# Kernel tuning notes

Hardware: AMD Instinct MI355X
Metric: run time of the kernel (lower is better)

## Reference

```python
import jax, jax.numpy as jnp
import numpy as np

B, PS, E, A, EMB, D, V, LC, TCAP = 128, 14, 2048, 512, 512, 512, 10000, 128, 26
T = TCAP - 1  # max decode length


def setup_inputs() -> dict:
    key = jax.random.key(0)
    ks = jax.random.split(key, 16)
    g = lambda k, shape: jax.random.normal(k, shape, jnp.float32) * 0.02
    cap_len = jax.random.randint(ks[2], (B, 1), 2, TCAP + 1).at[0, 0].set(TCAP)
    return {
        "encoder_out": jax.random.normal(ks[0], (B, PS, PS, E), jnp.float32),
        "encoded_captions": jax.random.randint(ks[1], (B, TCAP), 0, V),
        "caption_lengths": cap_len,
        "length_class": jax.random.randint(ks[3], (B,), 0, 3),
        "W_enc_att": g(ks[4], (E, A)), "b_enc_att": jnp.zeros((A,), jnp.float32),
        "W_dec_att": g(ks[5], (D, A)), "b_dec_att": jnp.zeros((A,), jnp.float32),
        "w_full_att": g(ks[6], (A,)), "b_full_att": jnp.zeros((), jnp.float32),
        "W_init_h": g(ks[7], (E, D)), "b_init_h": jnp.zeros((D,), jnp.float32),
        "W_init_c": g(ks[8], (E, D)), "b_init_c": jnp.zeros((D,), jnp.float32),
        "W_fbeta": g(ks[9], (D, E)), "b_fbeta": jnp.zeros((E,), jnp.float32),
        "emb_table": jax.random.uniform(ks[10], (V, EMB), jnp.float32, -0.1, 0.1),
        "lc_table": jax.random.uniform(ks[11], (3, LC), jnp.float32, -0.1, 0.1),
        "W_fc": jax.random.uniform(ks[12], (D, V), jnp.float32, -0.1, 0.1),
        "b_fc": jnp.zeros((V,), jnp.float32),
        "W_ih": g(ks[13], (EMB + E + LC, 4 * D)), "b_ih": jnp.zeros((4 * D,), jnp.float32),
        "W_hh": g(ks[14], (D, 4 * D)), "b_hh": jnp.zeros((4 * D,), jnp.float32),
    }


def reference(encoder_out, encoded_captions, caption_lengths, length_class,
              W_enc_att, b_enc_att, W_dec_att, b_dec_att, w_full_att, b_full_att,
              W_init_h, b_init_h, W_init_c, b_init_c, W_fbeta, b_fbeta,
              emb_table, lc_table, W_fc, b_fc, W_ih, b_ih, W_hh, b_hh):
    enc = encoder_out.reshape(B, -1, E)                      # [B, P, E]
    cap_len = caption_lengths[:, 0]
    sort_ind = jnp.argsort(-cap_len)                          # descending by length
    enc = enc[sort_ind]
    caps = encoded_captions[sort_ind]
    style = lc_table[length_class[sort_ind]]                  # [B, LC]
    dec_len = cap_len[sort_ind] - 1                           # [B]

    embs = emb_table[caps]                                    # [B, TCAP, EMB]
    mean_enc = enc.mean(axis=1)
    h0 = mean_enc @ W_init_h + b_init_h
    c0 = mean_enc @ W_init_c + b_init_c
    # encoder side of attention is time-invariant: precompute once
    att1 = jnp.einsum('bpe,ea->bpa', enc, W_enc_att) + b_enc_att

    def step(carry, xs):
        h, c = carry
        t, emb_t = xs
        att2 = h @ W_dec_att + b_dec_att
        e = jnp.einsum('bpa,a->bp', jax.nn.relu(att1 + att2[:, None, :]), w_full_att) + b_full_att
        alpha = jax.nn.softmax(e, axis=1)                     # [B, P]
        awe = jnp.einsum('bpe,bp->be', enc, alpha)
        gate = jax.nn.sigmoid(h @ W_fbeta + b_fbeta)
        x = jnp.concatenate([emb_t, style, gate * awe], axis=1)
        gates = x @ W_ih + b_ih + h @ W_hh + b_hh             # [B, 4D], order i,f,g,o
        i, f, g, o = jnp.split(gates, 4, axis=1)
        c_new = jax.nn.sigmoid(f) * c + jax.nn.sigmoid(i) * jnp.tanh(g)
        h_new = jax.nn.sigmoid(o) * jnp.tanh(c_new)
        preds = h_new @ W_fc + b_fc                           # dropout is identity in eval
        m = (t < dec_len)[:, None]                            # active sequences at step t
        return ((jnp.where(m, h_new, h), jnp.where(m, c_new, c)),
                (jnp.where(m, preds, 0.0), jnp.where(m, alpha, 0.0)))

    ts = jnp.arange(T)
    emb_seq = jnp.swapaxes(embs[:, :T, :], 0, 1)              # [T, B, EMB]
    _, (preds, alphas) = jax.lax.scan(step, (h0, c0), (ts, emb_seq))
    predictions = jnp.swapaxes(preds, 0, 1)                   # [B, T, V]
    alphas = jnp.swapaxes(alphas, 0, 1)                       # [B, T, P]
    return predictions, caps, dec_len, alphas, sort_ind
```

## Files before the change

kernel.cpp:

```cpp
#include <hip/hip_runtime.h>
#include <math.h>

constexpr int kB   = 128;
constexpr int kP   = 196;
constexpr int kE   = 2048;
constexpr int kA   = 512;
constexpr int kEMB = 512;
constexpr int kD   = 512;
constexpr int kV   = 10000;
constexpr int kLC  = 128;
constexpr int kTCAP= 26;
constexpr int kT   = 25;
constexpr int kX   = kEMB + kLC + kE;
constexpr int kXH  = kX + kD;
constexpr int kN3  = kV + kA + kE;
constexpr int kBIG = 1 << 30;
constexpr int KZ   = 5;

typedef __attribute__((ext_vector_type(8))) short bf8;
typedef __attribute__((ext_vector_type(4))) float f4;

__device__ inline float b2f(ushort u) { return __uint_as_float(((unsigned)u) << 16); }
__device__ inline ushort f2b(float f) {
    unsigned u = __float_as_uint(f);
    return (ushort)((u + 0x7fffu + ((u >> 16) & 1u)) >> 16);
}

#define SWZ(r, k) ((((r) * 32) + (k)) ^ (((r) & 7) << 3))

__global__ __launch_bounds__(128) void sort_setup(
    const int* __restrict__ caplen, const int* __restrict__ caps_in,
    const int* __restrict__ lclass, const float* __restrict__ lc_table,
    int* __restrict__ sort_ind, int* __restrict__ declen, int* __restrict__ caps_i,
    float* __restrict__ style,
    float* __restrict__ out_caps, float* __restrict__ out_declen,
    float* __restrict__ out_sortind)
{
    __shared__ int lens[kB];
    __shared__ int sind[kB];
    int i = threadIdx.x;
    lens[i] = caplen[i];
    __syncthreads();
    int li = lens[i];
    int r = 0;
    for (int j = 0; j < kB; j++) {
        int lj = lens[j];
        if (lj > li || (lj == li && j < i)) r++;
    }
    sind[r] = i;
    sort_ind[r] = i;
    out_sortind[r] = (float)i;
    __syncthreads();
    int orig = sind[i];
    int dl = lens[orig] - 1;
    declen[i] = dl;
    out_declen[i] = (float)dl;
    for (int t = 0; t < kTCAP; t++) {
        int cv = caps_in[orig * kTCAP + t];
        caps_i[i * kTCAP + t] = cv;
        out_caps[i * kTCAP + t] = (float)cv;
    }
    int lcl = lclass[orig];
    for (int k = 0; k < kLC; k++) style[i * kLC + k] = lc_table[lcl * kLC + k];
}

__global__ __launch_bounds__(256) void tcvt_kernel(
    const float* __restrict__ src, int ldsrc, int K, int N,
    ushort* __restrict__ dst, long long ldd)
{
    __shared__ float tile[32][33];
    int k0 = blockIdx.y * 32, n0 = blockIdx.x * 32;
    int tx = threadIdx.x & 31, ty = threadIdx.x >> 5;
    #pragma unroll
    for (int j = 0; j < 4; j++) {
        int k = k0 + ty + j * 8, n = n0 + tx;
        tile[ty + j * 8][tx] = (k < K && n < N) ? src[(long long)k * ldsrc + n] : 0.f;
    }
    __syncthreads();
    #pragma unroll
    for (int j = 0; j < 4; j++) {
        int n = n0 + ty + j * 8, k = k0 + tx;
        if (n < N && k < K) dst[(long long)n * ldd + k] = f2b(tile[tx][ty + j * 8]);
    }
}

__global__ __launch_bounds__(256) void bias_setup_kernel(
    const float* __restrict__ b_fc, const float* __restrict__ b_dec,
    const float* __restrict__ b_fb, const float* __restrict__ b_ih0,
    const float* __restrict__ b_ic0, const float* __restrict__ b_ih,
    const float* __restrict__ b_hh,
    float* __restrict__ bias3, float* __restrict__ bias_hc, float* __restrict__ gbias)
{
    int idx = blockIdx.x * 256 + threadIdx.x;
    if (idx < kN3) {
        float v;
        if (idx < kV) v = b_fc[idx];
        else if (idx < kV + kA) v = b_dec[idx - kV];
        else v = b_fb[idx - kV - kA];
        bias3[idx] = v;
    } else if (idx < kN3 + 1024) {
        int i = idx - kN3;
        bias_hc[i] = (i < 512) ? b_ih0[i] : b_ic0[i - 512];
    } else if (idx < kN3 + 1024 + 2048) {
        int i = idx - kN3 - 1024;
        gbias[i] = b_ih[i] + b_hh[i];
    }
}

__global__ __launch_bounds__(256) void enc_cvt_kernel(
    const float* __restrict__ enc, const int* __restrict__ sort_ind,
    ushort* __restrict__ enc_bf)
{
    long long idx4 = (long long)blockIdx.x * 256 + threadIdx.x;
    if (idx4 >= (long long)kB * kP * kE / 4) return;
    int r = (int)(idx4 >> 9);
    int cc = ((int)idx4 & 511) * 4;
    int b = r / kP, p = r - b * kP;
    long long srow = (long long)sort_ind[b] * kP + p;
    float4 v = *(const float4*)(enc + srow * kE + cc);
    ushort4 o; o.x = f2b(v.x); o.y = f2b(v.y); o.z = f2b(v.z); o.w = f2b(v.w);
    *(ushort4*)(enc_bf + (long long)r * kE + cc) = o;
}

__global__ __launch_bounds__(256) void mean_enc_kernel(
    const float* __restrict__ encf, const ushort* __restrict__ encb, int use_bf,
    const int* __restrict__ sort_ind, float* __restrict__ me)
{
    int idx = blockIdx.x * 256 + threadIdx.x;
    int b = idx >> 11, e = idx & 2047;
    float s = 0.f;
    if (use_bf) {
        const ushort* base = encb + (long long)b * kP * kE + e;
        #pragma unroll 4
        for (int p = 0; p < kP; p++) s += b2f(base[(long long)p * kE]);
    } else {
        const float* base = encf + (long long)sort_ind[b] * kP * kE + e;
        #pragma unroll 4
        for (int p = 0; p < kP; p++) s += base[(long long)p * kE];
    }
    me[idx] = s * (1.0f / 196.0f);
}

__global__ __launch_bounds__(256) void gemm2(
    const void* __restrict__ Am, int lda, int a_bf16,
    const ushort* __restrict__ Bt, int ldbt,
    const float* __restrict__ bias,
    void* __restrict__ out1, long long ldc1, int c1_bf16,
    int split1, float* __restrict__ out2, long long ldc2,
    int split2, float* __restrict__ out3, long long ldc3,
    const int* __restrict__ declen, int t, int pred_mode,
    int M, int N, int K, long long zstride)
{
    __shared__ short As[64 * 32];
    __shared__ short Bs[128 * 32];
    int tid = threadIdx.x;
    int lane = tid & 63, w = tid >> 6, quad = lane >> 4, l16 = lane & 15;
    int m0 = blockIdx.y * 64, n0 = blockIdx.x * 128;

    f4 acc[8];
    #pragma unroll
    for (int i = 0; i < 8; i++) acc[i] = (f4){0.f, 0.f, 0.f, 0.f};

    int a_r = tid >> 2;
    int a_kc = (tid & 3) * 8;
    long long a_row = m0 + a_r;
    const float*  a_srcf = (const float*)Am  + a_row * (long long)lda + a_kc;
    const ushort* a_srcb = (const ushort*)Am + a_row * (long long)lda + a_kc;

    int b_r = tid >> 1;
    int b_kc = (tid & 1) * 16;
    bool bvalid = (n0 + b_r) < N;
    const ushort* b_src = Bt + (long long)(n0 + b_r) * ldbt + b_kc;

    int kpb = K / (int)gridDim.z;
    int kbeg = (int)blockIdx.z * kpb, kend = kbeg + kpb;

    float4 af0 = make_float4(0.f, 0.f, 0.f, 0.f), af1 = af0;
    uint4 au, bu0, bu1;
    au.x = au.y = au.z = au.w = 0u; bu0 = au; bu1 = au;

    if (a_bf16) au = *(const uint4*)(a_srcb + kbeg);
    else { af0 = *(const float4*)(a_srcf + kbeg); af1 = *(const float4*)(a_srcf + kbeg + 4); }
    if (bvalid) { bu0 = *(const uint4*)(b_src + kbeg); bu1 = *(const uint4*)(b_src + kbeg + 8); }

    for (int k0 = kbeg; k0 < kend; k0 += 32) {
        __syncthreads();
        if (a_bf16) {
            *(uint4*)&As[SWZ(a_r, a_kc)] = au;
        } else {
            uint4 pk; ushort* pp = (ushort*)&pk;
            pp[0] = f2b(af0.x); pp[1] = f2b(af0.y); pp[2] = f2b(af0.z); pp[3] = f2b(af0.w);
            pp[4] = f2b(af1.x); pp[5] = f2b(af1.y); pp[6] = f2b(af1.z); pp[7] = f2b(af1.w);
            *(uint4*)&As[SWZ(a_r, a_kc)] = pk;
        }
        *(uint4*)&Bs[SWZ(b_r, b_kc)]     = bu0;
        *(uint4*)&Bs[SWZ(b_r, b_kc + 8)] = bu1;
        int kn = k0 + 32;
        if (kn < kend) {
            if (a_bf16) au = *(const uint4*)(a_srcb + kn);
            else { af0 = *(const float4*)(a_srcf + kn); af1 = *(const float4*)(a_srcf + kn + 4); }
            if (bvalid) { bu0 = *(const uint4*)(b_src + kn); bu1 = *(const uint4*)(b_src + kn + 8); }
        }
        __syncthreads();
        bf8 a = *(const bf8*)&As[SWZ(w * 16 + l16, quad * 8)];
        #pragma unroll
        for (int nt = 0; nt < 8; nt++) {
            bf8 b = *(const bf8*)&Bs[SWZ(nt * 16 + l16, quad * 8)];
            acc[nt] = __builtin_amdgcn_mfma_f32_16x16x32_bf16(a, b, acc[nt], 0, 0, 0);
        }
    }

    long long zoff = (long long)blockIdx.z * zstride;
    #pragma unroll
    for (int nt = 0; nt < 8; nt++) {
        int cn = n0 + nt * 16 + l16;
        if (cn >= N) continue;
        float bv = bias ? bias[cn] : 0.f;
        #pragma unroll
        for (int reg = 0; reg < 4; reg++) {
            int rr = m0 + w * 16 + quad * 4 + reg;
            float v = acc[nt][reg] + bv;
            if (cn < split1) {
                long long idx;
                if (pred_mode) {
                    int bb = rr & 127, tt = rr >> 7;
                    if (tt >= declen[bb]) v = 0.f;
                    idx = ((long long)bb * kT + tt) * ldc1 + cn;
                } else {
                    if (declen && t >= declen[rr]) v = 0.f;
                    idx = (long long)rr * ldc1 + cn + zoff;
                }
                if (c1_bf16) ((ushort*)out1)[idx] = f2b(v);
                else         ((float*)out1)[idx] = v;
            } else if (cn < split2) {
                out2[(long long)rr * ldc2 + (cn - split1)] = v;
            } else {
                out3[(long long)rr * ldc3 + (cn - split2)] = v;
            }
        }
    }
}

__global__ __launch_bounds__(256) void gemm_big(
    const ushort* __restrict__ A, int lda,
    const ushort* __restrict__ Bt, int ldbt,
    const float* __restrict__ bias,
    void* __restrict__ out1, long long ldc1, int c1_bf16,
    const int* __restrict__ declen, int pred_mode,
    int M, int N, int K)
{
    __shared__ short As[128 * 32];
    __shared__ short Bs[128 * 32];
    unsigned nwg = gridDim.x * gridDim.y;
    unsigned lin = blockIdx.y * gridDim.x + blockIdx.x;
    unsigned q = nwg >> 3, rm = nwg & 7;
    unsigned xcd = lin & 7, loc = lin >> 3;
    unsigned swz = (xcd < rm ? xcd * (q + 1) : rm * (q + 1) + (xcd - rm) * q) + loc;
    int bx = (int)(swz % gridDim.x), by = (int)(swz / gridDim.x);
    int m0 = by * 128, n0 = bx * 128;

    int tid = threadIdx.x;
    int lane = tid & 63, w = tid >> 6, quad = lane >> 4, l16 = lane & 15;
    int wr = w >> 1, wc = w & 1;

    f4 acc[4][4];
    #pragma unroll
    for (int m = 0; m < 4; m++)
        #pragma unroll
        for (int n = 0; n < 4; n++) acc[m][n] = (f4){0.f, 0.f, 0.f, 0.f};

    bool wact = true;
    if (pred_mode) wact = declen[wr * 64] > (m0 >> 7);

    int s_r = tid >> 1, s_kc = (tid & 1) * 16;
    const ushort* a_src = A + (long long)(m0 + s_r) * lda + s_kc;
    bool bval = (n0 + s_r) < N;
    const ushort* b_src = Bt + (long long)(n0 + s_r) * ldbt + s_kc;

    uint4 au0, au1, bu0, bu1;
    au0.x = au0.y = au0.z = au0.w = 0u; au1 = au0; bu0 = au0; bu1 = au0;
    au0 = *(const uint4*)(a_src);
    au1 = *(const uint4*)(a_src + 8);
    if (bval) { bu0 = *(const uint4*)(b_src); bu1 = *(const uint4*)(b_src + 8); }

    for (int k0 = 0; k0 < K; k0 += 32) {
        __syncthreads();
        *(uint4*)&As[SWZ(s_r, s_kc)]     = au0;
        *(uint4*)&As[SWZ(s_r, s_kc + 8)] = au1;
        *(uint4*)&Bs[SWZ(s_r, s_kc)]     = bu0;
        *(uint4*)&Bs[SWZ(s_r, s_kc + 8)] = bu1;
        int kn = k0 + 32;
        if (kn < K) {
            au0 = *(const uint4*)(a_src + kn);
            au1 = *(const uint4*)(a_src + kn + 8);
            if (bval) { bu0 = *(const uint4*)(b_src + kn); bu1 = *(const uint4*)(b_src + kn + 8); }
        }
        __syncthreads();
        if (wact) {
            bf8 af[4], bfr[4];
            #pragma unroll
            for (int m = 0; m < 4; m++)
                af[m] = *(const bf8*)&As[SWZ(wr * 64 + m * 16 + l16, quad * 8)];
            #pragma unroll
            for (int n = 0; n < 4; n++)
                bfr[n] = *(const bf8*)&Bs[SWZ(wc * 64 + n * 16 + l16, quad * 8)];
            #pragma unroll
            for (int m = 0; m < 4; m++)
                #pragma unroll
                for (int n = 0; n < 4; n++)
                    acc[m][n] = __builtin_amdgcn_mfma_f32_16x16x32_bf16(af[m], bfr[n], acc[m][n], 0, 0, 0);
        }
    }

    #pragma unroll
    for (int n = 0; n < 4; n++) {
        int cn = n0 + wc * 64 + n * 16 + l16;
        if (cn >= N) continue;
        float bv = bias ? bias[cn] : 0.f;
        #pragma unroll
        for (int m = 0; m < 4; m++) {
            #pragma unroll
            for (int reg = 0; reg < 4; reg++) {
                int rr = m0 + wr * 64 + m * 16 + quad * 4 + reg;
                float v = acc[m][n][reg] + bv;
                long long idx;
                if (pred_mode) {
                    int bb = rr & 127, tt = rr >> 7;
                    if (tt >= declen[bb]) v = 0.f;
                    idx = ((long long)bb * kT + tt) * ldc1 + cn;
                } else {
                    idx = (long long)rr * ldc1 + cn;
                }
                if (c1_bf16) ((ushort*)out1)[idx] = f2b(v);
                else         ((float*)out1)[idx] = v;
            }
        }
    }
}

__global__ __launch_bounds__(512) void attn_awe_kernel(
    const ushort* __restrict__ att1, const float* __restrict__ att2,
    const float* __restrict__ w_full, const float* __restrict__ b_full,
    const float* __restrict__ encf, const ushort* __restrict__ encb, int use_bf,
    const int* __restrict__ sort_ind, const float* __restrict__ gate,
    const int* __restrict__ caps_i, int t,
    const float* __restrict__ emb_table, const float* __restrict__ style,
    float* __restrict__ xh, float* __restrict__ alphas_out,
    const int* __restrict__ declen, const int* __restrict__ smap)
{
    int b = blockIdx.y;
    int half = blockIdx.x;
    int ob = smap ? smap[b] : b;
    __shared__ float al[kP];
    __shared__ float red1[8], red2[8];
    int tid = threadIdx.x, wave = tid >> 6, lane = tid & 63;

    float a2r[8], wfr[8];
    {
        const float4* ap = (const float4*)(att2 + (long long)b * kA + lane * 8);
        *(float4*)&a2r[0] = ap[0]; *(float4*)&a2r[4] = ap[1];
        const float4* wp = (const float4*)(w_full + lane * 8);
        *(float4*)&wfr[0] = wp[0]; *(float4*)&wfr[4] = wp[1];
    }
    float bfull = b_full[0];
    const ushort* a1 = att1 + (long long)ob * kP * kA + lane * 8;
    for (int i0 = 0; i0 < 25; i0 += 4) {
        uint4 u[4]; int pv[4];
        #pragma unroll
        for (int j = 0; j < 4; j++) {
            int i = i0 + j, p = wave + 8 * i;
            pv[j] = (i < 25 && p < kP) ? p : -1;
            if (pv[j] >= 0) u[j] = *(const uint4*)(a1 + (long long)pv[j] * kA);
        }
        #pragma unroll
        for (int j = 0; j < 4; j++) {
            if (pv[j] < 0) continue;
            const unsigned* uw = (const unsigned*)&u[j];
            float s = 0.f;
            #pragma unroll
            for (int q = 0; q < 4; q++) {
                unsigned x = uw[q];
                float v0 = b2f((ushort)(x & 0xffffu)) + a2r[2 * q];
                float v1 = b2f((ushort)(x >> 16))     + a2r[2 * q + 1];
                s += fmaxf(v0, 0.f) * wfr[2 * q] + fmaxf(v1, 0.f) * wfr[2 * q + 1];
            }
            #pragma unroll
            for (int off = 32; off; off >>= 1) s += __shfl_down(s, off);
            if (lane == 0) al[pv[j]] = s + bfull;
        }
    }
    __syncthreads();

    float e = (tid < kP) ? al[tid] : -1e30f;
    float wm = e;
    for (int off = 32; off; off >>= 1) wm = fmaxf(wm, __shfl_down(wm, off));
    if (lane == 0) red1[wave] = wm;
    __syncthreads();
    float gm = red1[0];
    #pragma unroll
    for (int i = 1; i < 8; i++) gm = fmaxf(gm, red1[i]);
    float ex = (tid < kP) ? expf(e - gm) : 0.f;
    float sw = ex;
    for (int off = 32; off; off >>= 1) sw += __shfl_down(sw, off);
    if (lane == 0) red2[wave] = sw;
    __syncthreads();
    float S = red2[0];
    #pragma unroll
    for (int i = 1; i < 8; i++) S += red2[i];
    float a = ex / S;
    __syncthreads();
    if (tid < kP) {
        al[tid] = a;
        if (half == 0)
            alphas_out[((long long)b * kT + t) * kP + tid] = (t < declen[b]) ? a : 0.f;
    }
    __syncthreads();

    if (half == 1 && tid < 160) {
        int tok = caps_i[b * kTCAP + t];
        float4 v;
        if (tid < 128) v = *(const float4*)(emb_table + (long long)tok * kEMB + tid * 4);
        else           v = *(const float4*)(style + b * kLC + (tid - 128) * 4);
        *(float4*)(xh + (long long)b * kXH + tid * 4) = v;
    }

    int c0 = half * 1024 + tid * 2;
    float s0 = 0.f, s1 = 0.f;
    if (use_bf) {
        const ushort* base = encb + (long long)b * kP * kE + c0;
        #pragma unroll 4
        for (int p = 0; p < kP; p++) {
            unsigned uu = *(const unsigned*)(base + (long long)p * kE);
            float ap = al[p];
            s0 += b2f((ushort)(uu & 0xffffu)) * ap;
            s1 += b2f((ushort)(uu >> 16))     * ap;
        }
    } else {
        const float* base = encf + (long long)sort_ind[b] * kP * kE + c0;
        #pragma unroll 4
        for (int p = 0; p < kP; p++) {
            float2 v = *(const float2*)(base + (long long)p * kE);
            float ap = al[p];
            s0 += v.x * ap; s1 += v.y * ap;
        }
    }
    float2 g = *(const float2*)(gate + (long long)b * kE + c0);
    float2 o;
    o.x = s0 / (1.f + expf(-g.x));
    o.y = s1 / (1.f + expf(-g.y));
    *(float2*)(xh + (long long)b * kXH + kEMB + kLC + c0) = o;
}

__global__ __launch_bounds__(256) void lstm_cell_kernel(
    const float* __restrict__ gpart, const float* __restrict__ gbias,
    float* __restrict__ xh, float* __restrict__ c,
    ushort* __restrict__ Hbuf, int t)
{
    int idx = blockIdx.x * 256 + threadIdx.x;
    int b = idx >> 9, d = idx & 511;
    float gi = gbias[d], gf = gbias[kD + d], gg = gbias[2 * kD + d], go = gbias[3 * kD + d];
    const float* g = gpart + (long long)b * 4 * kD + d;
    #pragma unroll
    for (int z = 0; z < KZ; z++) {
        const float* gz = g + (long long)z * kB * 4 * kD;
        gi += gz[0]; gf += gz[kD]; gg += gz[2 * kD]; go += gz[3 * kD];
    }
    float si = 1.f / (1.f + expf(-gi));
    float sf = 1.f / (1.f + expf(-gf));
    float so = 1.f / (1.f + expf(-go));
    float cn = sf * c[idx] + si * tanhf(gg);
    float hn = so * tanhf(cn);
    c[idx] = cn;
    xh[(long long)b * kXH + kX + d] = hn;
    Hbuf[((long long)t * kB + b) * kD + d] = f2b(hn);
}

extern "C" void kernel_launch(void* const* d_in, const int* in_sizes, int n_in,
                              void* d_out, int out_size, void* d_ws, size_t ws_size,
                              hipStream_t stream)
{
    const float* encoder_out  = (const float*)d_in[0];
    const int*   enc_caps     = (const int*)  d_in[1];
    const int*   cap_lengths  = (const int*)  d_in[2];
    const int*   length_class = (const int*)  d_in[3];
    const float* W_enc_att = (const float*)d_in[4];
    const float* b_enc_att = (const float*)d_in[5];
    const float* W_dec_att = (const float*)d_in[6];
    const float* b_dec_att = (const float*)d_in[7];
    const float* w_full_att = (const float*)d_in[8];
    const float* b_full_att = (const float*)d_in[9];
    const float* W_init_h = (const float*)d_in[10];
    const float* b_init_h = (const float*)d_in[11];
    const float* W_init_c = (const float*)d_in[12];
    const float* b_init_c = (const float*)d_in[13];
    const float* W_fbeta  = (const float*)d_in[14];
    const float* b_fbeta  = (const float*)d_in[15];
    const float* emb_table = (const float*)d_in[16];
    const float* lc_table  = (const float*)d_in[17];
    const float* W_fc = (const float*)d_in[18];
    const float* b_fc = (const float*)d_in[19];
    const float* W_ih = (const float*)d_in[20];
    const float* b_ih = (const float*)d_in[21];
    const float* W_hh = (const float*)d_in[22];
    const float* b_hh = (const float*)d_in[23];

    float* out = (float*)d_out;
    float* o_pred    = out;
    float* o_caps    = out + (long long)kB * kT * kV;
    float* o_declen  = o_caps + kB * kTCAP;
    float* o_alpha   = o_declen + kB;
    float* o_sortind = o_alpha + (long long)kB * kT * kP;

    float* w = (float*)d_ws;
    float* xh       = w; w += kB * kXH;
    float* c        = w; w += kB * kD;
    float* att2     = w; w += kB * kA;
    float* gate     = w; w += kB * kE;
    float* mean_enc = w; w += kB * kE;
    float* gpart    = w; w += (long long)kB * 4 * kD * KZ;
    float* style    = w; w += kB * kLC;
    float* bias3    = w; w += kN3;
    float* bias_hc  = w; w += 1024;
    float* gbias    = w; w += 2048;
    ushort* us = (ushort*)w;
    ushort* att1_bf  = us; us += (long long)kB * kP * kA;
    ushort* WencT    = us; us += (long long)kA * kE;
    ushort* WhcT     = us; us += (long long)1024 * kE;
    ushort* WcatT    = us; us += (long long)(4 * kD) * kXH;
    ushort* Wcat3T   = us; us += (long long)kN3 * kD;
    ushort* Hbuf     = us; us += (long long)kT * kB * kD;
    int* iw = (int*)us;
    int* sort_ind = iw; iw += kB;
    int* declen   = iw; iw += kB;
    int* caps_i   = iw; iw += kB * kTCAP;
    ushort* enc_bf = (ushort*)(iw + kB);

    size_t need_with_enc = ((char*)(enc_bf + (long long)kB * kP * kE)) - (char*)d_ws;
    int use_encbf = (ws_size >= need_with_enc) ? 1 : 0;

    sort_setup<<<1, 128, 0, stream>>>(cap_lengths, enc_caps, length_class, lc_table,
        sort_ind, declen, caps_i, style, o_caps, o_declen, o_sortind);

    auto tc = [&](const float* s, int ldsrc, int Kr, int Nc, ushort* d, long long ldd) {
        tcvt_kernel<<<dim3((Nc + 31) / 32, (Kr + 31) / 32), 256, 0, stream>>>(
            s, ldsrc, Kr, Nc, d, ldd);
    };
    tc(W_enc_att, kA, kE, kA, WencT, kE);
    tc(W_init_h,  kD, kE, kD, WhcT, kE);
    tc(W_init_c,  kD, kE, kD, WhcT + (long long)kD * kE, kE);
    tc(W_ih, 4 * kD, kX, 4 * kD, WcatT, kXH);
    tc(W_hh, 4 * kD, kD, 4 * kD, WcatT + kX, kXH);
    tc(W_fc,      kV, kD, kV, Wcat3T, kD);
    tc(W_dec_att, kA, kD, kA, Wcat3T + (long long)kV * kD, kD);
    tc(W_fbeta,   kE, kD, kE, Wcat3T + (long long)(kV + kA) * kD, kD);
    bias_setup_kernel<<<(kN3 + 1024 + 2048 + 255) / 256, 256, 0, stream>>>(
        b_fc, b_dec_att, b_fbeta, b_init_h, b_init_c, b_ih, b_hh, bias3, bias_hc, gbias);

    if (use_encbf) {
        enc_cvt_kernel<<<(unsigned)(((long long)kB * kP * kE / 4 + 255) / 256), 256, 0, stream>>>(
            encoder_out, sort_ind, enc_bf);
    }
    mean_enc_kernel<<<(kB * kE) / 256, 256, 0, stream>>>(
        encoder_out, enc_bf, use_encbf, sort_ind, mean_enc);

    auto g2 = [](int M, int N) { return dim3((unsigned)((N + 127) / 128), (unsigned)(M / 64)); };

    gemm2<<<g2(kB, 1024), 256, 0, stream>>>(mean_enc, kE, 0, WhcT, kE, bias_hc,
        xh + kX, kXH, 0, 512, c, kD, kBIG, nullptr, 0, nullptr, 0, 0,
        kB, 1024, kE, 0);

    if (use_encbf) {
        gemm_big<<<dim3(kA / 128, kB * kP / 128), 256, 0, stream>>>(
            enc_bf, kE, WencT, kE, b_enc_att,
            att1_bf, kA, 1, nullptr, 0, kB * kP, kA, kE);
    } else {
        gemm2<<<g2(kB * kP, kA), 256, 0, stream>>>(encoder_out, kE, 0, WencT, kE, b_enc_att,
            att1_bf, kA, 1, kBIG, nullptr, 0, kBIG, nullptr, 0, nullptr, 0, 0,
            kB * kP, kA, kE, 0);
    }

    gemm2<<<g2(kB, kA + kE), 256, 0, stream>>>(xh + kX, kXH, 0,
        Wcat3T + (long long)kV * kD, kD, bias3 + kV, att2, kA, 0,
        kA, gate, kE, kBIG, nullptr, 0, nullptr, 0, 0, kB, kA + kE, kD, 0);

    const int* smap = use_encbf ? nullptr : sort_ind;
    for (int t = 0; t < kT; t++) {
        attn_awe_kernel<<<dim3(2, kB), 512, 0, stream>>>(att1_bf, att2, w_full_att,
            b_full_att, encoder_out, enc_bf, use_encbf, sort_ind, gate, caps_i, t,
            emb_table, style, xh, o_alpha, declen, smap);
        gemm2<<<dim3((4 * kD + 127) / 128, kB / 64, KZ), 256, 0, stream>>>(
            xh, kXH, 0, WcatT, kXH, nullptr,
            gpart, 4 * kD, 0, kBIG, nullptr, 0, kBIG, nullptr, 0, nullptr, 0, 0,
            kB, 4 * kD, kXH, (long long)kB * 4 * kD);
        lstm_cell_kernel<<<(kB * kD) / 256, 256, 0, stream>>>(gpart, gbias, xh, c, Hbuf, t);
        gemm2<<<g2(kB, kA + kE), 256, 0, stream>>>(xh + kX, kXH, 0,
            Wcat3T + (long long)kV * kD, kD, bias3 + kV, att2, kA, 0,
            kA, gate, kE, kBIG, nullptr, 0, nullptr, 0, 0, kB, kA + kE, kD, 0);
    }

    gemm_big<<<dim3((kV + 127) / 128, kT * kB / 128), 256, 0, stream>>>(
        Hbuf, kD, Wcat3T, kD, bias3,
        o_pred, kV, 0, declen, 1, kT * kB, kV, kD);
}
```

Baseline: 2.737 ms.

## Transpose bf16 encoder to P-contiguous layout and keep LSTM input in bf16

Adds a kernel that transposes the bf16 encoder features into a [B, E, P] layout padded to 200 so that the per-step attention-weighted sum and the mean reduction read contiguous 16-byte vectors instead of strided scalars. The xh activation buffer also becomes bf16, which halves the A-operand traffic for the recurrent gate GEMMs and drops the fp32-to-bf16 conversion there. In exchange the code spends an extra transpose pass and more workspace, falls back to the old paths when the workspace is too small, and rounds the hidden state to bf16 before the recurrent matmul.

Measured after the change: 2.634 ms. -3.8%, faster.

```diff
diff --git a/kernel.cpp b/kernel.cpp
--- a/kernel.cpp
+++ b/kernel.cpp
@@ -3,6 +3,7 @@
 
 constexpr int kB   = 128;
 constexpr int kP   = 196;
+constexpr int kPT  = 200;
 constexpr int kE   = 2048;
 constexpr int kA   = 512;
 constexpr int kEMB = 512;
@@ -122,14 +123,43 @@
     *(ushort4*)(enc_bf + (long long)r * kE + cc) = o;
 }
 
+__global__ __launch_bounds__(256) void encT_kernel(
+    const ushort* __restrict__ enc_bf, ushort* __restrict__ enc_T)
+{
+    __shared__ ushort tile[kPT][65];
+    int b = blockIdx.y, e0 = blockIdx.x * 64;
+    int tid = threadIdx.x;
+    tile[196 + (tid >> 6)][tid & 63] = 0;
+    const ushort* src = enc_bf + (long long)b * kP * kE + e0;
+    for (int idx = tid; idx < kP * 64; idx += 256) {
+        int p = idx >> 6, j = idx & 63;
+        tile[p][j] = src[(long long)p * kE + j];
+    }
+    __syncthreads();
+    ushort* dst = enc_T + ((long long)b * kE + e0) * kPT;
+    for (int j = 0; j < 64; j++) {
+        if (tid < kPT) dst[(long long)j * kPT + tid] = tile[tid][j];
+    }
+}
+
 __global__ __launch_bounds__(256) void mean_enc_kernel(
-    const float* __restrict__ encf, const ushort* __restrict__ encb, int use_bf,
+    const float* __restrict__ encf, const ushort* __restrict__ encb,
+    const ushort* __restrict__ encT, int mode,
     const int* __restrict__ sort_ind, float* __restrict__ me)
 {
     int idx = blockIdx.x * 256 + threadIdx.x;
     int b = idx >> 11, e = idx & 2047;
     float s = 0.f;
-    if (use_bf) {
+    if (mode == 2) {
+        const ushort* base = encT + (long long)idx * kPT;
+        #pragma unroll
+        for (int i = 0; i < kPT / 8; i++) {
+            uint4 u = *(const uint4*)(base + i * 8);
+            const ushort* pu = (const ushort*)&u;
+            #pragma unroll
+            for (int j = 0; j < 8; j++) s += b2f(pu[j]);
+        }
+    } else if (mode == 1) {
         const ushort* base = encb + (long long)b * kP * kE + e;
         #pragma unroll 4
         for (int p = 0; p < kP; p++) s += b2f(base[(long long)p * kE]);
@@ -341,17 +371,18 @@
 __global__ __launch_bounds__(512) void attn_awe_kernel(
     const ushort* __restrict__ att1, const float* __restrict__ att2,
     const float* __restrict__ w_full, const float* __restrict__ b_full,
-    const float* __restrict__ encf, const ushort* __restrict__ encb, int use_bf,
+    const float* __restrict__ encf, const ushort* __restrict__ encb,
+    const ushort* __restrict__ encT, int mode,
     const int* __restrict__ sort_ind, const float* __restrict__ gate,
     const int* __restrict__ caps_i, int t,
     const float* __restrict__ emb_table, const float* __restrict__ style,
-    float* __restrict__ xh, float* __restrict__ alphas_out,
+    ushort* __restrict__ xh, float* __restrict__ alphas_out,
     const int* __restrict__ declen, const int* __restrict__ smap)
 {
     int b = blockIdx.y;
     int half = blockIdx.x;
     int ob = smap ? smap[b] : b;
-    __shared__ float al[kP];
+    __shared__ float al[kPT];
     __shared__ float red1[8], red2[8];
     int tid = threadIdx.x, wave = tid >> 6, lane = tid & 63;
 
@@ -413,6 +444,8 @@
         al[tid] = a;
         if (half == 0)
             alphas_out[((long long)b * kT + t) * kP + tid] = (t < declen[b]) ? a : 0.f;
+    } else if (tid < kPT) {
+        al[tid] = 0.f;
     }
     __syncthreads();
 
@@ -421,12 +454,29 @@
         float4 v;
         if (tid < 128) v = *(const float4*)(emb_table + (long long)tok * kEMB + tid * 4);
         else           v = *(const float4*)(style + b * kLC + (tid - 128) * 4);
-        *(float4*)(xh + (long long)b * kXH + tid * 4) = v;
+        ushort4 o; o.x = f2b(v.x); o.y = f2b(v.y); o.z = f2b(v.z); o.w = f2b(v.w);
+        *(ushort4*)(xh + (long long)b * kXH + tid * 4) = o;
     }
 
     int c0 = half * 1024 + tid * 2;
     float s0 = 0.f, s1 = 0.f;
-    if (use_bf) {
+    if (mode == 2) {
+        const ushort* r0 = encT + ((long long)b * kE + c0) * kPT;
+        const ushort* r1 = r0 + kPT;
+        #pragma unroll 5
+        for (int i = 0; i < kPT / 8; i++) {
+            uint4 ua = *(const uint4*)(r0 + i * 8);
+            uint4 ub = *(const uint4*)(r1 + i * 8);
+            f4 alo = *(const f4*)&al[i * 8];
+            f4 ahi = *(const f4*)&al[i * 8 + 4];
+            const ushort* pa = (const ushort*)&ua;
+            const ushort* pb = (const ushort*)&ub;
+            s0 += b2f(pa[0]) * alo.x + b2f(pa[1]) * alo.y + b2f(pa[2]) * alo.z + b2f(pa[3]) * alo.w;
+            s0 += b2f(pa[4]) * ahi.x + b2f(pa[5]) * ahi.y + b2f(pa[6]) * ahi.z + b2f(pa[7]) * ahi.w;
+            s1 += b2f(pb[0]) * alo.x + b2f(pb[1]) * alo.y + b2f(pb[2]) * alo.z + b2f(pb[3]) * alo.w;
+            s1 += b2f(pb[4]) * ahi.x + b2f(pb[5]) * ahi.y + b2f(pb[6]) * ahi.z + b2f(pb[7]) * ahi.w;
+        }
+    } else if (mode == 1) {
         const ushort* base = encb + (long long)b * kP * kE + c0;
         #pragma unroll 4
         for (int p = 0; p < kP; p++) {
@@ -445,15 +495,15 @@
         }
     }
     float2 g = *(const float2*)(gate + (long long)b * kE + c0);
-    float2 o;
-    o.x = s0 / (1.f + expf(-g.x));
-    o.y = s1 / (1.f + expf(-g.y));
-    *(float2*)(xh + (long long)b * kXH + kEMB + kLC + c0) = o;
+    float o0 = s0 / (1.f + expf(-g.x));
+    float o1 = s1 / (1.f + expf(-g.y));
+    unsigned pw = (unsigned)f2b(o0) | ((unsigned)f2b(o1) << 16);
+    *(unsigned*)(xh + (long long)b * kXH + kEMB + kLC + c0) = pw;
 }
 
 __global__ __launch_bounds__(256) void lstm_cell_kernel(
     const float* __restrict__ gpart, const float* __restrict__ gbias,
-    float* __restrict__ xh, float* __restrict__ c,
+    ushort* __restrict__ xh, float* __restrict__ c,
     ushort* __restrict__ Hbuf, int t)
 {
     int idx = blockIdx.x * 256 + threadIdx.x;
@@ -471,8 +521,9 @@
     float cn = sf * c[idx] + si * tanhf(gg);
     float hn = so * tanhf(cn);
     c[idx] = cn;
-    xh[(long long)b * kXH + kX + d] = hn;
-    Hbuf[((long long)t * kB + b) * kD + d] = f2b(hn);
+    ushort hb = f2b(hn);
+    xh[(long long)b * kXH + kX + d] = hb;
+    Hbuf[((long long)t * kB + b) * kD + d] = hb;
 }
 
 extern "C" void kernel_launch(void* const* d_in, const int* in_sizes, int n_in,
@@ -512,7 +563,6 @@
     float* o_sortind = o_alpha + (long long)kB * kT * kP;
 
     float* w = (float*)d_ws;
-    float* xh       = w; w += kB * kXH;
     float* c        = w; w += kB * kD;
     float* att2     = w; w += kB * kA;
     float* gate     = w; w += kB * kE;
@@ -523,6 +573,7 @@
     float* bias_hc  = w; w += 1024;
     float* gbias    = w; w += 2048;
     ushort* us = (ushort*)w;
+    ushort* xh_bf    = us; us += (long long)kB * kXH;
     ushort* att1_bf  = us; us += (long long)kB * kP * kA;
     ushort* WencT    = us; us += (long long)kA * kE;
     ushort* WhcT     = us; us += (long long)1024 * kE;
@@ -534,9 +585,13 @@
     int* declen   = iw; iw += kB;
     int* caps_i   = iw; iw += kB * kTCAP;
     ushort* enc_bf = (ushort*)(iw + kB);
-
-    size_t need_with_enc = ((char*)(enc_bf + (long long)kB * kP * kE)) - (char*)d_ws;
-    int use_encbf = (ws_size >= need_with_enc) ? 1 : 0;
+    ushort* enc_T  = enc_bf + (long long)kB * kP * kE;
+
+    size_t need_encbf = ((char*)(enc_bf + (long long)kB * kP * kE)) - (char*)d_ws;
+    size_t need_encT  = ((char*)(enc_T  + (long long)kB * kE * kPT)) - (char*)d_ws;
+    int use_encbf = (ws_size >= need_encbf) ? 1 : 0;
+    int use_encT  = (ws_size >= need_encT) ? 1 : 0;
+    int mode = use_encT ? 2 : (use_encbf ? 1 : 0);
 
     sort_setup<<<1, 128, 0, stream>>>(cap_lengths, enc_caps, length_class, lc_table,
         sort_ind, declen, caps_i, style, o_caps, o_declen, o_sortind);
@@ -560,13 +615,16 @@
         enc_cvt_kernel<<<(unsigned)(((long long)kB * kP * kE / 4 + 255) / 256), 256, 0, stream>>>(
             encoder_out, sort_ind, enc_bf);
     }
+    if (use_encT) {
+        encT_kernel<<<dim3(kE / 64, kB), 256, 0, stream>>>(enc_bf, enc_T);
+    }
     mean_enc_kernel<<<(kB * kE) / 256, 256, 0, stream>>>(
-        encoder_out, enc_bf, use_encbf, sort_ind, mean_enc);
+        encoder_out, enc_bf, enc_T, mode, sort_ind, mean_enc);
 
     auto g2 = [](int M, int N) { return dim3((unsigned)((N + 127) / 128), (unsigned)(M / 64)); };
 
     gemm2<<<g2(kB, 1024), 256, 0, stream>>>(mean_enc, kE, 0, WhcT, kE, bias_hc,
-        xh + kX, kXH, 0, 512, c, kD, kBIG, nullptr, 0, nullptr, 0, 0,
+        xh_bf + kX, kXH, 1, 512, c, kD, kBIG, nullptr, 0, nullptr, 0, 0,
         kB, 1024, kE, 0);
 
     if (use_encbf) {
@@ -579,21 +637,21 @@
             kB * kP, kA, kE, 0);
     }
 
-    gemm2<<<g2(kB, kA + kE), 256, 0, stream>>>(xh + kX, kXH, 0,
+    gemm2<<<g2(kB, kA + kE), 256, 0, stream>>>(xh_bf + kX, kXH, 1,
         Wcat3T + (long long)kV * kD, kD, bias3 + kV, att2, kA, 0,
         kA, gate, kE, kBIG, nullptr, 0, nullptr, 0, 0, kB, kA + kE, kD, 0);
 
     const int* smap = use_encbf ? nullptr : sort_ind;
     for (int t = 0; t < kT; t++) {
         attn_awe_kernel<<<dim3(2, kB), 512, 0, stream>>>(att1_bf, att2, w_full_att,
-            b_full_att, encoder_out, enc_bf, use_encbf, sort_ind, gate, caps_i, t,
-            emb_table, style, xh, o_alpha, declen, smap);
+            b_full_att, encoder_out, enc_bf, enc_T, mode, sort_ind, gate, caps_i, t,
+            emb_table, style, xh_bf, o_alpha, declen, smap);
         gemm2<<<dim3((4 * kD + 127) / 128, kB / 64, KZ), 256, 0, stream>>>(
-            xh, kXH, 0, WcatT, kXH, nullptr,
+            xh_bf, kXH, 1, WcatT, kXH, nullptr,
             gpart, 4 * kD, 0, kBIG, nullptr, 0, kBIG, nullptr, 0, nullptr, 0, 0,
             kB, 4 * kD, kXH, (long long)kB * 4 * kD);
-        lstm_cell_kernel<<<(kB * kD) / 256, 256, 0, stream>>>(gpart, gbias, xh, c, Hbuf, t);
-        gemm2<<<g2(kB, kA + kE), 256, 0, stream>>>(xh + kX, kXH, 0,
+        lstm_cell_kernel<<<(kB * kD) / 256, 256, 0, stream>>>(gpart, gbias, xh_bf, c, Hbuf, t);
+        gemm2<<<g2(kB, kA + kE), 256, 0, stream>>>(xh_bf + kX, kXH, 1,
             Wcat3T + (long long)kV * kD, kD, bias3 + kV, att2, kA, 0,
             kA, gate, kE, kBIG, nullptr, 0, nullptr, 0, 0, kB, kA + kE, kD, 0);
     }
```
